# Optimization experiments

Measured on AMD Instinct MI355X. Metric: run time of the kernel, lower is better.

Reference implementation:

```python
import jax, jax.numpy as jnp
import numpy as np

B, T, D = 8, 512, 1024
H, DQK, DV = 16, 128, 128  # n_heads, d_qk = emb_dim//h_qk, d_v = emb_dim//h_v


def setup_inputs() -> dict:
    key = jax.random.key(0)
    ks = jax.random.split(key, 8)
    s = 0.02
    return {
        "X": jax.random.normal(ks[0], (B, T, D), jnp.float32),
        "pos_enc_k": jax.random.normal(ks[1], (T, T, DQK), jnp.float32) * s,
        "pos_enc_v": jax.random.normal(ks[2], (T, T, DV), jnp.float32) * s,
        "Wq": jax.random.normal(ks[3], (D, H * DQK), jnp.float32) * s,
        "bq": jnp.zeros((H * DQK,), jnp.float32),
        "Wk": jax.random.normal(ks[4], (D, H * DQK), jnp.float32) * s,
        "bk": jnp.zeros((H * DQK,), jnp.float32),
        "Wv": jax.random.normal(ks[5], (D, H * DV), jnp.float32) * s,
        "bv": jnp.zeros((H * DV,), jnp.float32),
        "Wp": jax.random.normal(ks[6], (H * DV, D), jnp.float32) * s,
        "bp": jnp.zeros((D,), jnp.float32),
    }


def reference(X, pos_enc_k, pos_enc_v, Wq, bq, Wk, bk, Wv, bv, Wp, bp):
    b, t, d = X.shape
    # projections -> (b, h, t, dhead)
    Q = (X @ Wq + bq).reshape(b, t, H, DQK).transpose(0, 2, 1, 3)
    K = (X @ Wk + bk).reshape(b, t, H, DQK).transpose(0, 2, 1, 3)
    V = (X @ Wv + bv).reshape(b, t, H, DV).transpose(0, 2, 1, 3)
    # content attention + relative-position key bias
    att = jnp.einsum("bhqd,bhkd->bhqk", Q, K)
    att = att + jnp.einsum("bhqd,qkd->bhqk", Q, pos_enc_k)
    att = att / jnp.sqrt(jnp.asarray(DQK, X.dtype))
    # causal mask (do_mask=True)
    causal = jnp.tril(jnp.ones((t, t), bool))
    att = jnp.where(causal[None, None], att, jnp.asarray(-jnp.inf, att.dtype))
    att = jax.nn.softmax(att, axis=-1)
    # values + relative-position value correction
    y = jnp.einsum("bhqk,bhkd->bhqd", att, V)
    y = y + jnp.einsum("bhqk,qkd->bhqd", att, pos_enc_v)
    y = y.transpose(0, 2, 1, 3).reshape(b, t, H * DV)
    return y @ Wp + bp
```

## Files before the change

kernel.cpp:

```cpp
#include <hip/hip_runtime.h>
#include <stdint.h>

#define B_  8
#define T_  512
#define D_  1024
#define H_  16
#define DH  128
#define BH  128
#define ND  2048
#define BT  4096

typedef __attribute__((ext_vector_type(8))) short          short8;
typedef __attribute__((ext_vector_type(8))) __bf16         bf16x8;
typedef __attribute__((ext_vector_type(4))) float          f32x4;
typedef __attribute__((ext_vector_type(4))) unsigned short ushort4v;

static __device__ __forceinline__ unsigned short f2bf(float f) {
  unsigned u = __builtin_bit_cast(unsigned, f);
  u += 0x7FFFu + ((u >> 16) & 1u);
  return (unsigned short)(u >> 16);
}
static __device__ __forceinline__ float bf2f(unsigned short h) {
  unsigned u = ((unsigned)h) << 16;
  return __builtin_bit_cast(float, u);
}
static __device__ __forceinline__ f32x4 mfma16(short8 a, short8 b, f32x4 c) {
  return __builtin_amdgcn_mfma_f32_16x16x32_bf16(
      __builtin_bit_cast(bf16x8, a), __builtin_bit_cast(bf16x8, b), c, 0, 0, 0);
}
static __device__ __forceinline__ void gload16(const unsigned short* g, unsigned short* l) {
  __builtin_amdgcn_global_load_lds(
      (const __attribute__((address_space(1))) void*)g,
      (__attribute__((address_space(3))) void*)l, 16, 0, 0);
}

template <int ROWS, int COLS>
static __device__ __forceinline__ void stage_gl2(unsigned short* lds,
                                                 const unsigned short* __restrict__ src,
                                                 long stride, int tid) {
  constexpr int CPR = COLS / 8;
#pragma unroll
  for (int it = 0; it < ROWS * COLS / 8 / 256; ++it) {
    int chunk = tid + it * 256;
    int r = chunk / CPR, c8 = (chunk % CPR) * 8;
    gload16(src + (long)r * stride + c8, lds + chunk * 8);
  }
}

template <int MR, int NR, int LDA, int LDB, int KD>
static __device__ __forceinline__ void mfma_blk(const unsigned short* As,
                                                const unsigned short* Bs,
                                                int a0, int b0, int lrow, int lk8,
                                                f32x4 (*acc)[NR]) {
#pragma unroll
  for (int ks = 0; ks < KD; ks += 32) {
    short8 a[MR], b[NR];
#pragma unroll
    for (int i = 0; i < MR; ++i) a[i] = *(const short8*)&As[(a0 + i * 16 + lrow) * LDA + ks + lk8];
#pragma unroll
    for (int j = 0; j < NR; ++j) b[j] = *(const short8*)&Bs[(b0 + j * 16 + lrow) * LDB + ks + lk8];
#pragma unroll
    for (int i = 0; i < MR; ++i)
#pragma unroll
      for (int j = 0; j < NR; ++j) acc[i][j] = mfma16(a[i], b[j], acc[i][j]);
  }
}

#define IDS4                             \
  const int tid  = threadIdx.x;          \
  const int lane = tid & 63;             \
  const int wid  = tid >> 6;             \
  const int lrow = lane & 15;            \
  const int lk8  = (lane >> 4) * 8;      \
  const int lr4  = (lane >> 4) * 4;      \
  const int wm = wid >> 1, wn = wid & 1;

#define LTS 132
#define LTQ 68

__global__ __launch_bounds__(256) void k_prep(const float* __restrict__ X,
                                              unsigned short* __restrict__ Xb,
                                              const float* __restrict__ Wq,
                                              const float* __restrict__ Wk,
                                              const float* __restrict__ Wv,
                                              const float* __restrict__ Wp,
                                              unsigned short* __restrict__ WT,
                                              unsigned short* __restrict__ WpT) {
  __shared__ float tile[32][33];
  int bid = blockIdx.x;
  if (bid < 4096) {
    int i = bid * 256 + threadIdx.x;
    f32x4 v = ((const f32x4*)X)[i];
    ushort4v o;
    o.x = f2bf(v.x); o.y = f2bf(v.y); o.z = f2bf(v.z); o.w = f2bf(v.w);
    ((ushort4v*)Xb)[i] = o;
    return;
  }
  bid -= 4096;
  const int which = bid >> 11;
  const int local = bid & 2047;
  const float* in;
  unsigned short* outp;
  int R, C, bx, by;
  if (which < 3) {
    in = which == 0 ? Wq : (which == 1 ? Wk : Wv);
    outp = WT + (size_t)which * ND * D_;
    R = D_; C = ND; bx = local & 63; by = local >> 6;
  } else {
    in = Wp; outp = WpT;
    R = ND; C = D_; bx = local & 31; by = local >> 5;
  }
  int c0 = bx * 32, r0 = by * 32;
  int tx = threadIdx.x & 31, ty = threadIdx.x >> 5;
#pragma unroll
  for (int i = 0; i < 32; i += 8)
    tile[ty + i][tx] = in[(long)(r0 + ty + i) * C + (c0 + tx)];
  __syncthreads();
#pragma unroll
  for (int i = 0; i < 32; i += 8)
    outp[(long)(c0 + ty + i) * R + (r0 + tx)] = f2bf(tile[tx][ty + i]);
}

__global__ __launch_bounds__(256) void k_vtrans(const unsigned short* __restrict__ vin,
                                                unsigned short* __restrict__ vout) {
  __shared__ unsigned short tile[32][33];
  int bh = blockIdx.z;
  int t0 = blockIdx.x * 32, d0 = blockIdx.y * 32;
  int tx = threadIdx.x & 31, ty = threadIdx.x >> 5;
#pragma unroll
  for (int i = 0; i < 32; i += 8)
    tile[ty + i][tx] = vin[((long)bh * T_ + t0 + ty + i) * DH + (d0 + tx)];
  __syncthreads();
#pragma unroll
  for (int i = 0; i < 32; i += 8)
    vout[((long)bh * DH + (d0 + ty + i)) * T_ + (t0 + tx)] = tile[tx][ty + i];
}

__global__ __launch_bounds__(512, 1) void k_proj8(const unsigned short* __restrict__ Xb,
                                                  const unsigned short* __restrict__ WT,
                                                  const float* __restrict__ bq,
                                                  const float* __restrict__ bk,
                                                  const float* __restrict__ bv,
                                                  unsigned short* __restrict__ Qb,
                                                  unsigned short* __restrict__ Kb,
                                                  unsigned short* __restrict__ Vb) {
  __shared__ unsigned short lds[3 * 24576];
  const int tid  = threadIdx.x;
  const int lane = tid & 63;
  const int wid  = tid >> 6;
  const int wm   = wid >> 2;
  const int wn   = wid & 3;
  const int lrow = lane & 15;
  const int lr4  = (lane >> 4) * 4;

  const int flat = blockIdx.x, xcd = flat & 7, local = flat >> 3;
  const int mt = (xcd & 1) * 16 + (local & 15);
  const int nt = (xcd >> 1) * 6 + (local >> 4);
  const int m0 = mt * 128, n0 = nt * 256;

  const unsigned short* Asrc = Xb + (long)m0 * D_;
  const unsigned short* Bsrc = WT + (long)n0 * D_;

  auto stageA = [&](int t) {
    unsigned short* base = lds + (t % 3) * 24576;
    const unsigned short* as = Asrc + t * 64;
#pragma unroll
    for (int it = 0; it < 2; ++it) {
      int n = tid + it * 512;
      int r = n >> 3, c = (n & 7) ^ (r & 7);
      gload16(as + (long)r * D_ + c * 8, base + n * 8);
    }
  };
  auto stageB1 = [&](int t) {
    unsigned short* base = lds + (t % 3) * 24576 + 8192;
    const unsigned short* bs = Bsrc + t * 64;
#pragma unroll
    for (int it = 0; it < 2; ++it) {
      int n = tid + it * 512;
      int r = n >> 3, c = (n & 7) ^ (r & 7);
      gload16(bs + (long)r * D_ + c * 8, base + n * 8);
    }
  };
  auto stageB2 = [&](int t) {
    unsigned short* base = lds + (t % 3) * 24576 + 8192;
    const unsigned short* bs = Bsrc + t * 64;
#pragma unroll
    for (int it = 2; it < 4; ++it) {
      int n = tid + it * 512;
      int r = n >> 3, c = (n & 7) ^ (r & 7);
      gload16(bs + (long)r * D_ + c * 8, base + n * 8);
    }
  };

  stageA(0); stageB1(0); stageB2(0);
  stageA(1); stageB1(1); stageB2(1);
  asm volatile("s_waitcnt vmcnt(6)" ::: "memory");
  __builtin_amdgcn_sched_barrier(0);
  __builtin_amdgcn_s_barrier();

  f32x4 acc[4][4] = {};
  for (int t = 0; t < 16; ++t) {
    const unsigned short* At = lds + (t % 3) * 24576;
    const unsigned short* Bt = At + 8192;
#pragma unroll
    for (int ph = 0; ph < 4; ++ph) {
      const int mh = ph >> 1, nh = ph & 1;
      short8 a[2][2], b[2][2];
#pragma unroll
      for (int i = 0; i < 2; ++i) {
        int ra = wm * 64 + mh * 32 + i * 16 + lrow;
#pragma unroll
        for (int ks = 0; ks < 2; ++ks) {
          int c = (ks * 4 + (lane >> 4)) ^ (ra & 7);
          a[i][ks] = *(const short8*)&At[ra * 64 + c * 8];
        }
      }
#pragma unroll
      for (int j = 0; j < 2; ++j) {
        int rb = wn * 64 + nh * 32 + j * 16 + lrow;
#pragma unroll
        for (int ks = 0; ks < 2; ++ks) {
          int c = (ks * 4 + (lane >> 4)) ^ (rb & 7);
          b[j][ks] = *(const short8*)&Bt[rb * 64 + c * 8];
        }
      }
      if (t < 14) {
        if (ph == 0) stageA(t + 2);
        else if (ph == 1) stageB1(t + 2);
        else if (ph == 2) stageB2(t + 2);
      }
      if (ph == 3) {
        if (t < 14) asm volatile("s_waitcnt vmcnt(6)" ::: "memory");
        else        asm volatile("s_waitcnt vmcnt(0)" ::: "memory");
        __builtin_amdgcn_sched_barrier(0);
      }
      __builtin_amdgcn_s_barrier();
      asm volatile("s_waitcnt lgkmcnt(0)" ::: "memory");
      __builtin_amdgcn_sched_barrier(0);
      __builtin_amdgcn_s_setprio(1);
#pragma unroll
      for (int ks = 0; ks < 2; ++ks)
#pragma unroll
        for (int i = 0; i < 2; ++i)
#pragma unroll
          for (int j = 0; j < 2; ++j)
            acc[mh * 2 + i][nh * 2 + j] =
                mfma16(a[i][ks], b[j][ks], acc[mh * 2 + i][nh * 2 + j]);
      __builtin_amdgcn_s_setprio(0);
      __builtin_amdgcn_s_barrier();
    }
  }

  const int nb = n0 >> 11;
  const float* biasp = nb == 0 ? bq : (nb == 1 ? bk : bv);
  unsigned short* dst = nb == 0 ? Qb : (nb == 1 ? Kb : Vb);
#pragma unroll
  for (int i = 0; i < 4; ++i)
#pragma unroll
    for (int j = 0; j < 4; ++j) {
      int c = (n0 & 2047) + wn * 64 + j * 16 + lrow;
      int h = c >> 7, dd = c & 127;
      float bias = biasp[c];
#pragma unroll
      for (int r = 0; r < 4; ++r) {
        int m = m0 + wm * 64 + i * 16 + lr4 + r;
        int bb = m >> 9, tt = m & (T_ - 1);
        dst[((long)(bb * H_ + h) * T_ + tt) * DH + dd] = f2bf(acc[i][j][r] + bias);
      }
    }
}

__global__ __launch_bounds__(256) void k_posk(const unsigned short* __restrict__ Qb,
                                              const float* __restrict__ Pk,
                                              unsigned short* __restrict__ att) {
  const int bid = blockIdx.x;
  const int q = (bid & 1) ? (T_ - 1 - (bid >> 1)) : (bid >> 1);
  const int ktiles = (q >> 6) + 1;
  __shared__ unsigned short As[128 * 128];
  __shared__ unsigned short Bs[2][64 * 136];
  IDS4
  stage_gl2<128, 128>(As, Qb + (long)q * DH, (long)T_ * DH, tid);
  f32x4 pv[8];
  const float* psrc = Pk + (long)q * T_ * DH;
  auto loadPk = [&](int kt) {
#pragma unroll
    for (int it = 0; it < 8; ++it) {
      int chunk = tid + it * 256;
      int r = chunk >> 5, c4 = (chunk & 31) * 4;
      pv[it] = *(const f32x4*)(psrc + (long)(kt * 64 + r) * DH + c4);
    }
  };
  auto writeB = [&](int buf) {
#pragma unroll
    for (int it = 0; it < 8; ++it) {
      int chunk = tid + it * 256;
      int r = chunk >> 5, c4 = (chunk & 31) * 4;
      ushort4v o;
      o.x = f2bf(pv[it].x); o.y = f2bf(pv[it].y); o.z = f2bf(pv[it].z); o.w = f2bf(pv[it].w);
      *(ushort4v*)&Bs[buf][r * 136 + c4] = o;
    }
  };
  loadPk(0);
  asm volatile("s_waitcnt vmcnt(0)" ::: "memory");
  writeB(0);
  asm volatile("s_waitcnt lgkmcnt(0)" ::: "memory");
  __builtin_amdgcn_s_barrier();
  for (int kt = 0; kt < ktiles; ++kt) {
    const bool pre = (kt + 1 < ktiles);
    if (pre) loadPk(kt + 1);
    f32x4 acc[4][2] = {};
    mfma_blk<4, 2, 128, 136, 128>(As, Bs[kt & 1], wm * 64, wn * 32, lrow, lk8, acc);
    if (pre) {
      asm volatile("s_waitcnt vmcnt(0)" ::: "memory");
      writeB((kt + 1) & 1);
    }
#pragma unroll
    for (int i = 0; i < 4; ++i)
#pragma unroll
      for (int j = 0; j < 2; ++j) {
        int k = kt * 64 + wn * 32 + j * 16 + lrow;
#pragma unroll
        for (int r = 0; r < 4; ++r) {
          int bh = wm * 64 + i * 16 + lr4 + r;
          att[((long)q * BH + bh) * T_ + k] = f2bf(acc[i][j][r]);
        }
      }
    asm volatile("s_waitcnt lgkmcnt(0)" ::: "memory");
    __builtin_amdgcn_s_barrier();
  }
}

__global__ __launch_bounds__(256) void k_qkv(const unsigned short* __restrict__ Qb,
                                             const unsigned short* __restrict__ Kb,
                                             const unsigned short* __restrict__ Vt,
                                             unsigned short* __restrict__ att,
                                             float* __restrict__ Sinv,
                                             unsigned short* __restrict__ Ybb) {
  const int bh = blockIdx.x & 127, pr = blockIdx.x >> 7;
  __shared__ unsigned short Qs[64 * 128], Ks[64 * 128], Vs[128 * 64];
  __shared__ unsigned short Ps[64 * 72];
  __shared__ float lt[64 * LTQ];
  __shared__ float sInv[64];
  const int tid = threadIdx.x;
  const int lane = tid & 63, wid = tid >> 6;
  const int wm = wid >> 1, wn = wid & 1;
  const int lrow = lane & 15, lk8 = (lane >> 4) * 8, lr4 = (lane >> 4) * 4;
  const int row = tid >> 2, c0 = (tid & 3) * 16;
  const float scale = 0.08838834764831845f;
  const int b = bh >> 4, h = bh & 15;

  for (int pass = 0; pass < 2; ++pass) {
    const int qt = pass ? 7 - pr : pr;
    const int q0 = qt * 64, ktiles = qt + 1;
    const int qabs = q0 + row;
    unsigned short* arow = att + ((long)qabs * BH + bh) * T_;
    {
      const unsigned short* src = Qb + ((long)bh * T_ + q0) * DH;
#pragma unroll
      for (int it = 0; it < 4; ++it) {
        int n = tid + it * 256;
        int r = n >> 4, c = (n & 15) ^ (r & 7);
        gload16(src + (long)r * DH + c * 8, Qs + n * 8);
      }
    }
    float ssum = 0.f;
    f32x4 accv[2][4] = {};
    for (int kt = 0; kt < ktiles; ++kt) {
      const unsigned short* ksrc = Kb + ((long)bh * T_ + kt * 64) * DH;
#pragma unroll
      for (int it = 0; it < 4; ++it) {
        int n = tid + it * 256;
        int r = n >> 4, c = (n & 15) ^ (r & 7);
        gload16(ksrc + (long)r * DH + c * 8, Ks + n * 8);
      }
      const unsigned short* vsrc = Vt + (long)bh * DH * T_ + kt * 64;
#pragma unroll
      for (int it = 0; it < 4; ++it) {
        int n = tid + it * 256;
        int r = n >> 3, c = (n & 7) ^ (r & 7);
        gload16(vsrc + (long)r * T_ + c * 8, Vs + n * 8);
      }
      short8 pb0 = *(const short8*)(arow + kt * 64 + c0);
      short8 pb1 = *(const short8*)(arow + kt * 64 + c0 + 8);
      __syncthreads();
      f32x4 acc[2][2] = {};
#pragma unroll
      for (int ks = 0; ks < 4; ++ks) {
        short8 aq[2], bk2[2];
#pragma unroll
        for (int i = 0; i < 2; ++i) {
          int ra = wm * 32 + i * 16 + lrow;
          int c = (ks * 4 + (lane >> 4)) ^ (ra & 7);
          aq[i] = *(const short8*)&Qs[ra * 128 + c * 8];
        }
#pragma unroll
        for (int j = 0; j < 2; ++j) {
          int rb = wn * 32 + j * 16 + lrow;
          int c = (ks * 4 + (lane >> 4)) ^ (rb & 7);
          bk2[j] = *(const short8*)&Ks[rb * 128 + c * 8];
        }
#pragma unroll
        for (int i = 0; i < 2; ++i)
#pragma unroll
          for (int j = 0; j < 2; ++j)
            acc[i][j] = mfma16(aq[i], bk2[j], acc[i][j]);
      }
#pragma unroll
      for (int i = 0; i < 2; ++i)
#pragma unroll
        for (int j = 0; j < 2; ++j)
#pragma unroll
          for (int r = 0; r < 4; ++r)
            lt[(wm * 32 + i * 16 + lr4 + r) * LTQ + wn * 32 + j * 16 + lrow] = acc[i][j][r];
      __syncthreads();
      short8 o0, o1;
#pragma unroll
      for (int jj = 0; jj < 8; ++jj) {
        int k = kt * 64 + c0 + jj;
        float e0 = (k <= qabs)
                   ? __expf((lt[row * LTQ + c0 + jj] + bf2f((unsigned short)pb0[jj])) * scale) : 0.f;
        float e1 = (k + 8 <= qabs)
                   ? __expf((lt[row * LTQ + c0 + 8 + jj] + bf2f((unsigned short)pb1[jj])) * scale) : 0.f;
        o0[jj] = (short)f2bf(e0);
        o1[jj] = (short)f2bf(e1);
        ssum += e0 + e1;
      }
      *(short8*)(arow + kt * 64 + c0) = o0;
      *(short8*)(arow + kt * 64 + c0 + 8) = o1;
      *(short8*)&Ps[row * 72 + c0] = o0;
      *(short8*)&Ps[row * 72 + c0 + 8] = o1;
      __syncthreads();
#pragma unroll
      for (int ks = 0; ks < 2; ++ks) {
        short8 ap[2], bv2[4];
#pragma unroll
        for (int i = 0; i < 2; ++i) {
          int ra = wm * 32 + i * 16 + lrow;
          ap[i] = *(const short8*)&Ps[ra * 72 + ks * 32 + lk8];
        }
#pragma unroll
        for (int j = 0; j < 4; ++j) {
          int rb = wn * 64 + j * 16 + lrow;
          int c = ((ks * 4) + (lane >> 4)) ^ (rb & 7);
          bv2[j] = *(const short8*)&Vs[rb * 64 + c * 8];
        }
#pragma unroll
        for (int i = 0; i < 2; ++i)
#pragma unroll
          for (int j = 0; j < 4; ++j)
            accv[i][j] = mfma16(ap[i], bv2[j], accv[i][j]);
      }
      __syncthreads();
    }
    ssum += __shfl_xor(ssum, 1, 64);
    ssum += __shfl_xor(ssum, 2, 64);
    float si = 1.f / ssum;
    if ((tid & 3) == 0) { sInv[row] = si; Sinv[(long)qabs * BH + bh] = si; }
    __syncthreads();
#pragma unroll
    for (int i = 0; i < 2; ++i) {
      float sc2[4];
#pragma unroll
      for (int r = 0; r < 4; ++r) sc2[r] = sInv[wm * 32 + i * 16 + lr4 + r];
#pragma unroll
      for (int j = 0; j < 4; ++j) {
        int d = wn * 64 + j * 16 + lrow;
#pragma unroll
        for (int r = 0; r < 4; ++r) {
          int q = q0 + wm * 32 + i * 16 + lr4 + r;
          Ybb[(long)(b * T_ + q) * ND + h * DH + d] = f2bf(accv[i][j][r] * sc2[r]);
        }
      }
    }
    __syncthreads();
  }
}

__global__ __launch_bounds__(256) void k_posv(const unsigned short* __restrict__ P,
                                              const float* __restrict__ Pv,
                                              const float* __restrict__ Sinv,
                                              unsigned short* __restrict__ Ybb) {
  const int bid = blockIdx.x;
  const int q = (bid & 1) ? (T_ - 1 - (bid >> 1)) : (bid >> 1);
  const int ktiles = (q >> 6) + 1;
  __shared__ unsigned short As[128 * 64];
  __shared__ unsigned short Bs[2][128 * 72];
  __shared__ float lt[64 * LTQ];
  IDS4
  f32x4 pv[8];
  const float* psrc = Pv + (long)q * T_ * DH;
  auto loadPv = [&](int kt) {
#pragma unroll
    for (int it = 0; it < 8; ++it) {
      int chunk = tid + it * 256;
      int d4 = (chunk & 3) * 4 + ((chunk >> 6) & 7) * 16;
      int k  = ((chunk >> 2) & 15) + ((chunk >> 9) & 3) * 16;
      pv[it] = *(const f32x4*)(psrc + (long)(kt * 64 + k) * DH + d4);
    }
  };
  auto writeB = [&](int buf) {
#pragma unroll
    for (int it = 0; it < 8; ++it) {
      int chunk = tid + it * 256;
      int d4 = (chunk & 3) * 4 + ((chunk >> 6) & 7) * 16;
      int k  = ((chunk >> 2) & 15) + ((chunk >> 9) & 3) * 16;
      Bs[buf][(d4 + 0) * 72 + k] = f2bf(pv[it].x);
      Bs[buf][(d4 + 1) * 72 + k] = f2bf(pv[it].y);
      Bs[buf][(d4 + 2) * 72 + k] = f2bf(pv[it].z);
      Bs[buf][(d4 + 3) * 72 + k] = f2bf(pv[it].w);
    }
  };
  loadPv(0);
  asm volatile("s_waitcnt vmcnt(0)" ::: "memory");
  writeB(0);
  asm volatile("s_waitcnt lgkmcnt(0)" ::: "memory");
  __builtin_amdgcn_s_barrier();
  f32x4 acc[4][4] = {};
  for (int kt = 0; kt < ktiles; ++kt) {
    const bool pre = (kt + 1 < ktiles);
    stage_gl2<128, 64>(As, P + (long)q * BH * T_ + kt * 64, T_, tid);
    if (pre) loadPv(kt + 1);
    if (pre) asm volatile("s_waitcnt vmcnt(8)" ::: "memory");
    else     asm volatile("s_waitcnt vmcnt(0)" ::: "memory");
    __builtin_amdgcn_s_barrier();
    mfma_blk<4, 4, 64, 72, 64>(As, Bs[kt & 1], wm * 64, wn * 64, lrow, lk8, acc);
    if (pre) {
      asm volatile("s_waitcnt vmcnt(0)" ::: "memory");
      writeB((kt + 1) & 1);
    }
    asm volatile("s_waitcnt lgkmcnt(0)" ::: "memory");
    __builtin_amdgcn_s_barrier();
  }
  const int row = tid >> 2, c0 = (tid & 3) * 16;
#pragma unroll
  for (int hb = 0; hb < 2; ++hb)
#pragma unroll
    for (int hd = 0; hd < 2; ++hd) {
      int bh = hb * 64 + row;
      long idx = ((long)((bh >> 4) * T_ + q)) * ND + (bh & 15) * DH + hd * 64 + c0;
      short8 y0 = *(const short8*)&Ybb[idx];
      short8 y1 = *(const short8*)&Ybb[idx + 8];
      float sc = Sinv[(long)q * BH + bh];
      if (wm == hb && wn == hd) {
#pragma unroll
        for (int i = 0; i < 4; ++i)
#pragma unroll
          for (int j = 0; j < 4; ++j)
#pragma unroll
            for (int r = 0; r < 4; ++r)
              lt[(i * 16 + lr4 + r) * LTQ + j * 16 + lrow] = acc[i][j][r];
      }
      __syncthreads();
      short8 o0, o1;
#pragma unroll
      for (int jj = 0; jj < 8; ++jj) {
        o0[jj] = (short)f2bf(lt[row * LTQ + c0 + jj] * sc + bf2f((unsigned short)y0[jj]));
        o1[jj] = (short)f2bf(lt[row * LTQ + c0 + 8 + jj] * sc + bf2f((unsigned short)y1[jj]));
      }
      *(short8*)&Ybb[idx] = o0;
      *(short8*)&Ybb[idx + 8] = o1;
      __syncthreads();
    }
}

__global__ __launch_bounds__(256) void k_oproj(const unsigned short* __restrict__ Ybb,
                                               const unsigned short* __restrict__ WpT,
                                               const float* __restrict__ bp,
                                               float* __restrict__ outp) {
  __shared__ unsigned short As[128 * 64], Bs[128 * 64];
  IDS4
  const int m0 = blockIdx.y * 128, n0 = blockIdx.x * 128;
  f32x4 acc[4][4] = {};
  for (int kk = 0; kk < ND; kk += 64) {
    stage_gl2<128, 64>(As, Ybb + (long)m0 * ND + kk, ND, tid);
    stage_gl2<128, 64>(Bs, WpT + (long)n0 * ND + kk, ND, tid);
    __syncthreads();
    mfma_blk<4, 4, 64, 64, 64>(As, Bs, wm * 64, wn * 64, lrow, lk8, acc);
    __syncthreads();
  }
  float* lt = (float*)As;
  const int row = tid >> 4, c8 = (tid & 15) * 8;
  f32x4 b0 = *(const f32x4*)(bp + n0 + c8);
  f32x4 b1 = *(const f32x4*)(bp + n0 + c8 + 4);
#pragma unroll
  for (int rr = 0; rr < 8; ++rr) {
    if (wm == (rr >> 2)) {
      const int ii = rr & 3;
#pragma unroll
      for (int j = 0; j < 4; ++j)
#pragma unroll
        for (int r = 0; r < 4; ++r)
          lt[(lr4 + r) * LTS + wn * 64 + j * 16 + lrow] = acc[ii][j][r];
    }
    __syncthreads();
    f32x4 v0 = *(const f32x4*)&lt[row * LTS + c8];
    f32x4 v1 = *(const f32x4*)&lt[row * LTS + c8 + 4];
    int m = m0 + rr * 16 + row;
    v0.x += b0.x; v0.y += b0.y; v0.z += b0.z; v0.w += b0.w;
    v1.x += b1.x; v1.y += b1.y; v1.z += b1.z; v1.w += b1.w;
    *(f32x4*)&outp[(long)m * D_ + n0 + c8] = v0;
    *(f32x4*)&outp[(long)m * D_ + n0 + c8 + 4] = v1;
    __syncthreads();
  }
}

extern "C" void kernel_launch(void* const* d_in, const int* in_sizes, int n_in,
                              void* d_out, int out_size, void* d_ws, size_t ws_size,
                              hipStream_t stream) {
  const float* X  = (const float*)d_in[0];
  const float* Pk = (const float*)d_in[1];
  const float* Pv = (const float*)d_in[2];
  const float* Wq = (const float*)d_in[3];
  const float* bq = (const float*)d_in[4];
  const float* Wk = (const float*)d_in[5];
  const float* bk = (const float*)d_in[6];
  const float* Wv = (const float*)d_in[7];
  const float* bv = (const float*)d_in[8];
  const float* Wp = (const float*)d_in[9];
  const float* bp = (const float*)d_in[10];
  float* out = (float*)d_out;

  uint8_t* w = (uint8_t*)d_ws;
  unsigned short* Xb  = (unsigned short*)w; w += (size_t)BT * D_ * 2;
  unsigned short* WT  = (unsigned short*)w; w += (size_t)3 * ND * D_ * 2;
  unsigned short* WpT = (unsigned short*)w; w += (size_t)D_ * ND * 2;
  unsigned short* Qb  = (unsigned short*)w; w += (size_t)BH * T_ * DH * 2;
  unsigned short* Kb  = (unsigned short*)w; w += (size_t)BH * T_ * DH * 2;
  unsigned short* Vb  = (unsigned short*)w; w += (size_t)BH * T_ * DH * 2;
  unsigned short* Vt  = (unsigned short*)w; w += (size_t)BH * DH * T_ * 2;
  unsigned short* att = (unsigned short*)w; w += (size_t)T_ * BH * T_ * 2;
  unsigned short* Ybb = (unsigned short*)w; w += (size_t)BT * ND * 2;
  float*          Sinv= (float*)w;          w += (size_t)T_ * BH * 4;

  k_prep<<<12288, 256, 0, stream>>>(X, Xb, Wq, Wk, Wv, Wp, WT, WpT);
  k_proj8<<<768, 512, 0, stream>>>(Xb, WT, bq, bk, bv, Qb, Kb, Vb);
  k_vtrans<<<dim3(T_ / 32, DH / 32, BH), 256, 0, stream>>>(Vb, Vt);
  k_posk<<<T_, 256, 0, stream>>>(Qb, Pk, att);
  k_qkv<<<512, 256, 0, stream>>>(Qb, Kb, Vt, att, Sinv, Ybb);
  k_posv<<<T_, 256, 0, stream>>>(att, Pv, Sinv, Ybb);
  k_oproj<<<dim3(D_ / 128, BT / 128), 256, 0, stream>>>(Ybb, WpT, bp, out);
}
```

Before: 254.8 us.

## Enlarge QKV projection tiles to 256x256 and XOR-swizzle LDS in attention/oproj

The QKV projection kernel moves from 128x256 tiles with a triple-buffered, phase-interleaved load schedule to 256x256 tiles with double buffering. Each wave now holds 8x4 accumulators, which halves the block count and raises reuse per loaded tile. Separately, the pos_k, pos_v and output projection kernels switch their A-operand LDS staging to an XOR-swizzled layout to cut bank conflicts on LDS reads. The trade-offs are more register pressure and fewer blocks (384) in the projection, plus a coarser prefetch overlap than the old schedule.

```diff
diff --git a/kernel.cpp b/kernel.cpp
--- a/kernel.cpp
+++ b/kernel.cpp
@@ -34,31 +34,38 @@
       (__attribute__((address_space(3))) void*)l, 16, 0, 0);
 }
 
-template <int ROWS, int COLS>
-static __device__ __forceinline__ void stage_gl2(unsigned short* lds,
-                                                 const unsigned short* __restrict__ src,
-                                                 long stride, int tid) {
-  constexpr int CPR = COLS / 8;
-#pragma unroll
-  for (int it = 0; it < ROWS * COLS / 8 / 256; ++it) {
-    int chunk = tid + it * 256;
-    int r = chunk / CPR, c8 = (chunk % CPR) * 8;
-    gload16(src + (long)r * stride + c8, lds + chunk * 8);
-  }
-}
-
-template <int MR, int NR, int LDA, int LDB, int KD>
-static __device__ __forceinline__ void mfma_blk(const unsigned short* As,
-                                                const unsigned short* Bs,
-                                                int a0, int b0, int lrow, int lk8,
-                                                f32x4 (*acc)[NR]) {
-#pragma unroll
-  for (int ks = 0; ks < KD; ks += 32) {
+template <int ROWS>
+static __device__ __forceinline__ void stage_sw64(unsigned short* lds,
+                                                  const unsigned short* __restrict__ src,
+                                                  long stride, int tid) {
+#pragma unroll
+  for (int it = 0; it < ROWS / 32; ++it) {
+    int n = tid + it * 256;
+    int r = n >> 3, c = (n & 7) ^ (r & 7);
+    gload16(src + (long)r * stride + c * 8, lds + n * 8);
+  }
+}
+
+template <int MR, int NR>
+static __device__ __forceinline__ void mfma_sw64(const unsigned short* As,
+                                                 const unsigned short* Bs,
+                                                 int a0, int b0, int lrow, int g,
+                                                 f32x4 (*acc)[NR]) {
+#pragma unroll
+  for (int ks = 0; ks < 2; ++ks) {
     short8 a[MR], b[NR];
 #pragma unroll
-    for (int i = 0; i < MR; ++i) a[i] = *(const short8*)&As[(a0 + i * 16 + lrow) * LDA + ks + lk8];
-#pragma unroll
-    for (int j = 0; j < NR; ++j) b[j] = *(const short8*)&Bs[(b0 + j * 16 + lrow) * LDB + ks + lk8];
+    for (int i = 0; i < MR; ++i) {
+      int ra = a0 + i * 16 + lrow;
+      int c = (ks * 4 + g) ^ (ra & 7);
+      a[i] = *(const short8*)&As[ra * 64 + c * 8];
+    }
+#pragma unroll
+    for (int j = 0; j < NR; ++j) {
+      int rb = b0 + j * 16 + lrow;
+      int c = (ks * 4 + g) ^ (rb & 7);
+      b[j] = *(const short8*)&Bs[rb * 64 + c * 8];
+    }
 #pragma unroll
     for (int i = 0; i < MR; ++i)
 #pragma unroll
@@ -73,6 +80,7 @@
   const int lrow = lane & 15;            \
   const int lk8  = (lane >> 4) * 8;      \
   const int lr4  = (lane >> 4) * 4;      \
+  const int lg   = lane >> 4;            \
   const int wm = wid >> 1, wn = wid & 1;
 
 #define LTS 132
@@ -144,108 +152,79 @@
                                                   unsigned short* __restrict__ Qb,
                                                   unsigned short* __restrict__ Kb,
                                                   unsigned short* __restrict__ Vb) {
-  __shared__ unsigned short lds[3 * 24576];
+  __shared__ unsigned short lds[65536];
   const int tid  = threadIdx.x;
   const int lane = tid & 63;
+  const int g    = lane >> 4;
   const int wid  = tid >> 6;
   const int wm   = wid >> 2;
   const int wn   = wid & 3;
   const int lrow = lane & 15;
-  const int lr4  = (lane >> 4) * 4;
+  const int lr4  = g * 4;
 
   const int flat = blockIdx.x, xcd = flat & 7, local = flat >> 3;
-  const int mt = (xcd & 1) * 16 + (local & 15);
-  const int nt = (xcd >> 1) * 6 + (local >> 4);
-  const int m0 = mt * 128, n0 = nt * 256;
+  const int mt = local & 15;
+  const int nt = xcd * 3 + (local >> 4);
+  const int m0 = mt * 256, n0 = nt * 256;
 
   const unsigned short* Asrc = Xb + (long)m0 * D_;
   const unsigned short* Bsrc = WT + (long)n0 * D_;
 
-  auto stageA = [&](int t) {
-    unsigned short* base = lds + (t % 3) * 24576;
+  auto stage = [&](int t) {
+    unsigned short* base = lds + (t & 1) * 32768;
     const unsigned short* as = Asrc + t * 64;
-#pragma unroll
-    for (int it = 0; it < 2; ++it) {
+    const unsigned short* bs = Bsrc + t * 64;
+#pragma unroll
+    for (int it = 0; it < 4; ++it) {
       int n = tid + it * 512;
       int r = n >> 3, c = (n & 7) ^ (r & 7);
       gload16(as + (long)r * D_ + c * 8, base + n * 8);
     }
-  };
-  auto stageB1 = [&](int t) {
-    unsigned short* base = lds + (t % 3) * 24576 + 8192;
-    const unsigned short* bs = Bsrc + t * 64;
-#pragma unroll
-    for (int it = 0; it < 2; ++it) {
+#pragma unroll
+    for (int it = 0; it < 4; ++it) {
       int n = tid + it * 512;
       int r = n >> 3, c = (n & 7) ^ (r & 7);
-      gload16(bs + (long)r * D_ + c * 8, base + n * 8);
+      gload16(bs + (long)r * D_ + c * 8, base + 16384 + n * 8);
     }
   };
-  auto stageB2 = [&](int t) {
-    unsigned short* base = lds + (t % 3) * 24576 + 8192;
-    const unsigned short* bs = Bsrc + t * 64;
-#pragma unroll
-    for (int it = 2; it < 4; ++it) {
-      int n = tid + it * 512;
-      int r = n >> 3, c = (n & 7) ^ (r & 7);
-      gload16(bs + (long)r * D_ + c * 8, base + n * 8);
-    }
-  };
-
-  stageA(0); stageB1(0); stageB2(0);
-  stageA(1); stageB1(1); stageB2(1);
-  asm volatile("s_waitcnt vmcnt(6)" ::: "memory");
-  __builtin_amdgcn_sched_barrier(0);
-  __builtin_amdgcn_s_barrier();
-
-  f32x4 acc[4][4] = {};
+
+  stage(0);
+  f32x4 acc[8][4] = {};
   for (int t = 0; t < 16; ++t) {
-    const unsigned short* At = lds + (t % 3) * 24576;
-    const unsigned short* Bt = At + 8192;
-#pragma unroll
-    for (int ph = 0; ph < 4; ++ph) {
-      const int mh = ph >> 1, nh = ph & 1;
-      short8 a[2][2], b[2][2];
-#pragma unroll
-      for (int i = 0; i < 2; ++i) {
-        int ra = wm * 64 + mh * 32 + i * 16 + lrow;
-#pragma unroll
-        for (int ks = 0; ks < 2; ++ks) {
-          int c = (ks * 4 + (lane >> 4)) ^ (ra & 7);
-          a[i][ks] = *(const short8*)&At[ra * 64 + c * 8];
-        }
-      }
-#pragma unroll
-      for (int j = 0; j < 2; ++j) {
-        int rb = wn * 64 + nh * 32 + j * 16 + lrow;
-#pragma unroll
-        for (int ks = 0; ks < 2; ++ks) {
-          int c = (ks * 4 + (lane >> 4)) ^ (rb & 7);
-          b[j][ks] = *(const short8*)&Bt[rb * 64 + c * 8];
-        }
-      }
-      if (t < 14) {
-        if (ph == 0) stageA(t + 2);
-        else if (ph == 1) stageB1(t + 2);
-        else if (ph == 2) stageB2(t + 2);
-      }
-      if (ph == 3) {
-        if (t < 14) asm volatile("s_waitcnt vmcnt(6)" ::: "memory");
-        else        asm volatile("s_waitcnt vmcnt(0)" ::: "memory");
-        __builtin_amdgcn_sched_barrier(0);
-      }
-      __builtin_amdgcn_s_barrier();
+    const unsigned short* At = lds + (t & 1) * 32768;
+    const unsigned short* Bt = At + 16384;
+    if (t < 15) {
+      stage(t + 1);
+      asm volatile("s_waitcnt vmcnt(8)" ::: "memory");
+    } else {
+      asm volatile("s_waitcnt vmcnt(0)" ::: "memory");
+    }
+    __builtin_amdgcn_sched_barrier(0);
+    __builtin_amdgcn_s_barrier();
+#pragma unroll
+    for (int p = 0; p < 4; ++p) {
+      const int mh = p & 1, ks = p >> 1;
+      short8 a[4], b[4];
+#pragma unroll
+      for (int i = 0; i < 4; ++i) {
+        int ra = wm * 128 + mh * 64 + i * 16 + lrow;
+        int c = (ks * 4 + g) ^ (ra & 7);
+        a[i] = *(const short8*)&At[ra * 64 + c * 8];
+      }
+#pragma unroll
+      for (int j = 0; j < 4; ++j) {
+        int rb = wn * 64 + j * 16 + lrow;
+        int c = (ks * 4 + g) ^ (rb & 7);
+        b[j] = *(const short8*)&Bt[rb * 64 + c * 8];
+      }
       asm volatile("s_waitcnt lgkmcnt(0)" ::: "memory");
       __builtin_amdgcn_sched_barrier(0);
       __builtin_amdgcn_s_setprio(1);
 #pragma unroll
-      for (int ks = 0; ks < 2; ++ks)
-#pragma unroll
-        for (int i = 0; i < 2; ++i)
-#pragma unroll
-          for (int j = 0; j < 2; ++j)
-            acc[mh * 2 + i][nh * 2 + j] =
-                mfma16(a[i][ks], b[j][ks], acc[mh * 2 + i][nh * 2 + j]);
+      for (int i = 0; i < 4; ++i)
+#pragma unroll
+        for (int j = 0; j < 4; ++j)
+          acc[mh * 4 + i][j] = mfma16(a[i], b[j], acc[mh * 4 + i][j]);
       __builtin_amdgcn_s_setprio(0);
       __builtin_amdgcn_s_barrier();
     }
@@ -255,15 +234,15 @@
   const float* biasp = nb == 0 ? bq : (nb == 1 ? bk : bv);
   unsigned short* dst = nb == 0 ? Qb : (nb == 1 ? Kb : Vb);
 #pragma unroll
-  for (int i = 0; i < 4; ++i)
+  for (int i = 0; i < 8; ++i)
 #pragma unroll
     for (int j = 0; j < 4; ++j) {
-      int c = (n0 & 2047) + wn * 64 + j * 16 + lrow;
-      int h = c >> 7, dd = c & 127;
-      float bias = biasp[c];
+      int cc = (n0 & 2047) + wn * 64 + j * 16 + lrow;
+      int h = cc >> 7, dd = cc & 127;
+      float bias = biasp[cc];
 #pragma unroll
       for (int r = 0; r < 4; ++r) {
-        int m = m0 + wm * 64 + i * 16 + lr4 + r;
+        int m = m0 + wm * 128 + i * 16 + lr4 + r;
         int bb = m >> 9, tt = m & (T_ - 1);
         dst[((long)(bb * H_ + h) * T_ + tt) * DH + dd] = f2bf(acc[i][j][r] + bias);
       }
@@ -279,7 +258,15 @@
   __shared__ unsigned short As[128 * 128];
   __shared__ unsigned short Bs[2][64 * 136];
   IDS4
-  stage_gl2<128, 128>(As, Qb + (long)q * DH, (long)T_ * DH, tid);
+  {
+    const unsigned short* src = Qb + (long)q * DH;
+#pragma unroll
+    for (int it = 0; it < 8; ++it) {
+      int n = tid + it * 256;
+      int r = n >> 4, c = (n & 15) ^ (r & 7);
+      gload16(src + (long)r * (T_ * DH) + c * 8, As + n * 8);
+    }
+  }
   f32x4 pv[8];
   const float* psrc = Pk + (long)q * T_ * DH;
   auto loadPk = [&](int kt) {
@@ -309,7 +296,24 @@
     const bool pre = (kt + 1 < ktiles);
     if (pre) loadPk(kt + 1);
     f32x4 acc[4][2] = {};
-    mfma_blk<4, 2, 128, 136, 128>(As, Bs[kt & 1], wm * 64, wn * 32, lrow, lk8, acc);
+#pragma unroll
+    for (int ks = 0; ks < 4; ++ks) {
+      short8 a[4], b[2];
+#pragma unroll
+      for (int i = 0; i < 4; ++i) {
+        int ra = wm * 64 + i * 16 + lrow;
+        int c = (ks * 4 + lg) ^ (ra & 7);
+        a[i] = *(const short8*)&As[ra * 128 + c * 8];
+      }
+#pragma unroll
+      for (int j = 0; j < 2; ++j)
+        b[j] = *(const short8*)&Bs[kt & 1][(wn * 32 + j * 16 + lrow) * 136 + ks * 32 + lk8];
+#pragma unroll
+      for (int i = 0; i < 4; ++i)
+#pragma unroll
+        for (int j = 0; j < 2; ++j)
+          acc[i][j] = mfma16(a[i], b[j], acc[i][j]);
+    }
     if (pre) {
       asm volatile("s_waitcnt vmcnt(0)" ::: "memory");
       writeB((kt + 1) & 1);
@@ -518,12 +522,29 @@
   f32x4 acc[4][4] = {};
   for (int kt = 0; kt < ktiles; ++kt) {
     const bool pre = (kt + 1 < ktiles);
-    stage_gl2<128, 64>(As, P + (long)q * BH * T_ + kt * 64, T_, tid);
+    stage_sw64<128>(As, P + (long)q * BH * T_ + kt * 64, T_, tid);
     if (pre) loadPv(kt + 1);
     if (pre) asm volatile("s_waitcnt vmcnt(8)" ::: "memory");
     else     asm volatile("s_waitcnt vmcnt(0)" ::: "memory");
     __builtin_amdgcn_s_barrier();
-    mfma_blk<4, 4, 64, 72, 64>(As, Bs[kt & 1], wm * 64, wn * 64, lrow, lk8, acc);
+#pragma unroll
+    for (int ks = 0; ks < 2; ++ks) {
+      short8 a[4], b[4];
+#pragma unroll
+      for (int i = 0; i < 4; ++i) {
+        int ra = wm * 64 + i * 16 + lrow;
+        int c = (ks * 4 + lg) ^ (ra & 7);
+        a[i] = *(const short8*)&As[ra * 64 + c * 8];
+      }
+#pragma unroll
+      for (int j = 0; j < 4; ++j)
+        b[j] = *(const short8*)&Bs[kt & 1][(wn * 64 + j * 16 + lrow) * 72 + ks * 32 + lk8];
+#pragma unroll
+      for (int i = 0; i < 4; ++i)
+#pragma unroll
+        for (int j = 0; j < 4; ++j)
+          acc[i][j] = mfma16(a[i], b[j], acc[i][j]);
+    }
     if (pre) {
       asm volatile("s_waitcnt vmcnt(0)" ::: "memory");
       writeB((kt + 1) & 1);
@@ -572,10 +593,10 @@
   const int m0 = blockIdx.y * 128, n0 = blockIdx.x * 128;
   f32x4 acc[4][4] = {};
   for (int kk = 0; kk < ND; kk += 64) {
-    stage_gl2<128, 64>(As, Ybb + (long)m0 * ND + kk, ND, tid);
-    stage_gl2<128, 64>(Bs, WpT + (long)n0 * ND + kk, ND, tid);
+    stage_sw64<128>(As, Ybb + (long)m0 * ND + kk, ND, tid);
+    stage_sw64<128>(Bs, WpT + (long)n0 * ND + kk, ND, tid);
     __syncthreads();
-    mfma_blk<4, 4, 64, 64, 64>(As, Bs, wm * 64, wn * 64, lrow, lk8, acc);
+    mfma_sw64<4, 4>(As, Bs, wm * 64, wn * 64, lrow, lg, acc);
     __syncthreads();
   }
   float* lt = (float*)As;
@@ -633,7 +654,7 @@
   float*          Sinv= (float*)w;          w += (size_t)T_ * BH * 4;
 
   k_prep<<<12288, 256, 0, stream>>>(X, Xb, Wq, Wk, Wv, Wp, WT, WpT);
-  k_proj8<<<768, 512, 0, stream>>>(Xb, WT, bq, bk, bv, Qb, Kb, Vb);
+  k_proj8<<<384, 512, 0, stream>>>(Xb, WT, bq, bk, bv, Qb, Kb, Vb);
   k_vtrans<<<dim3(T_ / 32, DH / 32, BH), 256, 0, stream>>>(Vb, Vt);
   k_posk<<<T_, 256, 0, stream>>>(Qb, Pk, att);
   k_qkv<<<512, 256, 0, stream>>>(Qb, Kb, Vt, att, Sinv, Ybb);
```

New measurement: 248.3 us. 2.6% less time.
